# Kernel optimization log

Hardware: AMD Instinct MI355X
Metric: run time of the kernel (lower is better)

Reference implementation:

```python
import jax, jax.numpy as jnp
import numpy as np

D_MODEL = 256
N_HEADS = 8
D_FFN = 1024
B, N = 4, 1024
HEAD_DIM = D_MODEL // N_HEADS
LN_EPS = 1e-5


def _ln(x, g, b):
    mu = jnp.mean(x, axis=-1, keepdims=True)
    var = jnp.var(x, axis=-1, keepdims=True)
    return (x - mu) * jax.lax.rsqrt(var + LN_EPS) * g + b


def setup_inputs() -> dict:
    key = jax.random.key(0)
    ks = jax.random.split(key, 16)
    s = 0.02
    return {
        "embed": jax.random.normal(ks[0], (B, N, D_MODEL), jnp.float32),
        "refer_bbox": jax.random.uniform(ks[1], (B, N, 4), jnp.float32),
        "dist": jax.random.uniform(ks[2], (B, N, N), jnp.float32),
        "query_pos": jax.random.normal(ks[3], (B, N, D_MODEL), jnp.float32),
        "in_proj_w": jax.random.normal(ks[4], (3 * D_MODEL, D_MODEL), jnp.float32) * s,
        "in_proj_b": jnp.zeros((3 * D_MODEL,), jnp.float32),
        "out_w": jax.random.normal(ks[5], (D_MODEL, D_MODEL), jnp.float32) * s,
        "out_b": jnp.zeros((D_MODEL,), jnp.float32),
        "tau_w": jax.random.normal(ks[6], (N_HEADS, D_MODEL), jnp.float32) * s,
        "tau_b": jax.random.uniform(ks[7], (N_HEADS,), jnp.float32, 0.0, 2.0),
        "w1": jax.random.normal(ks[8], (D_FFN, D_MODEL), jnp.float32) * s,
        "b1": jnp.zeros((D_FFN,), jnp.float32),
        "w2": jax.random.normal(ks[9], (D_MODEL, D_FFN), jnp.float32) * s,
        "b2": jnp.zeros((D_MODEL,), jnp.float32),
        "g1": jnp.ones((D_MODEL,), jnp.float32),
        "beta1": jnp.zeros((D_MODEL,), jnp.float32),
        "g2": jnp.ones((D_MODEL,), jnp.float32),
        "beta2": jnp.zeros((D_MODEL,), jnp.float32),
    }


def reference(embed, refer_bbox, dist, query_pos, in_proj_w, in_proj_b, out_w, out_b,
              tau_w, tau_b, w1, b1, w2, b2, g1, beta1, g2, beta2):
    # tau: (B, N, H) -> (B, H, N); additive bias mask[b,h,i,j] = dist[b,i,j] * tau[b,h,i]
    tau = (embed @ tau_w.T + tau_b).transpose(0, 2, 1)
    bias = dist[:, None, :, :] * tau[..., None]  # (B, H, N, N)

    qk = embed + query_pos  # q = k = embed + pos, v = embed
    wq, wk, wv = jnp.split(in_proj_w, 3, axis=0)
    bq, bk, bv = jnp.split(in_proj_b, 3, axis=0)
    q = (qk @ wq.T + bq).reshape(B, N, N_HEADS, HEAD_DIM)
    k = (qk @ wk.T + bk).reshape(B, N, N_HEADS, HEAD_DIM)
    v = (embed @ wv.T + bv).reshape(B, N, N_HEADS, HEAD_DIM)

    scores = jnp.einsum("bihd,bjhd->bhij", q, k) / np.sqrt(HEAD_DIM) + bias
    attn = jax.nn.softmax(scores, axis=-1)
    ctx = jnp.einsum("bhij,bjhd->bihd", attn, v).reshape(B, N, D_MODEL)
    tgt = ctx @ out_w.T + out_b

    x = _ln(embed + tgt, g1, beta1)
    ffn = jax.nn.relu(x @ w1.T + b1) @ w2.T + b2
    return _ln(x + ffn, g2, beta2)
```

## Files before the change

kernel.cpp:

```cpp
#include <hip/hip_runtime.h>
#include <math.h>

#define D_MODEL 256
#define N_HEADS 8
#define HEAD_DIM 32
#define D_FFN   1024
#define BB      4
#define NN      1024
#define M_TOT   (BB * NN)
#define LN_EPS  1e-5f

#define QSCALE_LOG2E 0.2550348612f
#define LOG2E        1.4426950408889634f

typedef float f32x4 __attribute__((ext_vector_type(4)));
typedef short bf16x8 __attribute__((ext_vector_type(8)));

__device__ __forceinline__ unsigned short f2bf(float f) {
    unsigned int u = __float_as_uint(f);
    unsigned int r = (u + 0x7fffu + ((u >> 16) & 1u)) >> 16;
    return (unsigned short)r;
}
__device__ __forceinline__ ushort4 pack4(float4 v) {
    ushort4 o; o.x = f2bf(v.x); o.y = f2bf(v.y); o.z = f2bf(v.z); o.w = f2bf(v.w);
    return o;
}
__device__ __forceinline__ float fast_exp2(float x) {
#if __has_builtin(__builtin_amdgcn_exp2f)
    return __builtin_amdgcn_exp2f(x);
#else
    return exp2f(x);
#endif
}
__device__ __forceinline__ float bf2f(unsigned short s) {
    return __uint_as_float(((unsigned int)s) << 16);
}

__global__ __launch_bounds__(256)
void prep_all_kernel(const float4* __restrict__ e, const float4* __restrict__ qp,
                     ushort4* __restrict__ ebf, ushort4* __restrict__ qkbf,
                     const float4* __restrict__ inw, const float4* __restrict__ outw,
                     const float4* __restrict__ w1, const float4* __restrict__ w2,
                     const float4* __restrict__ tauw,
                     ushort4* __restrict__ o_inw, ushort4* __restrict__ o_outw,
                     ushort4* __restrict__ o_w1, ushort4* __restrict__ o_w2,
                     ushort4* __restrict__ o_taupad) {
    if (blockIdx.x < 1024) {
        int i = blockIdx.x * 256 + threadIdx.x;
        float4 ev = e[i], pv = qp[i];
        ebf[i] = pack4(ev);
        float4 s = make_float4(ev.x + pv.x, ev.y + pv.y, ev.z + pv.z, ev.w + pv.w);
        qkbf[i] = pack4(s);
    } else {
        int i = (blockIdx.x - 1024) * 256 + threadIdx.x;
        if (i < 49152)       o_inw[i] = pack4(inw[i]);
        else if (i < 65536)  o_outw[i - 49152] = pack4(outw[i - 49152]);
        else if (i < 131072) o_w1[i - 65536] = pack4(w1[i - 65536]);
        else if (i < 196608) o_w2[i - 131072] = pack4(w2[i - 131072]);
        else if (i < 200704) {
            int q = i - 196608;
            if (q < 512) o_taupad[q] = pack4(tauw[q]);
            else { ushort4 z = {0, 0, 0, 0}; o_taupad[q] = z; }
        }
    }
}

__global__ __launch_bounds__(256)
void qkv_mfma_kernel(const unsigned short* __restrict__ qk_bf,
                     const unsigned short* __restrict__ emb_bf,
                     const unsigned short* __restrict__ inw_bf,
                     const unsigned short* __restrict__ taupad,
                     const float* __restrict__ in_proj_b, const float* __restrict__ tau_b,
                     unsigned short* __restrict__ qb, unsigned short* __restrict__ kb,
                     unsigned short* __restrict__ vbT, float* __restrict__ taub) {
    __shared__ unsigned short vt[64][72];
    const int w    = threadIdx.x >> 6;
    const int lane = threadIdx.x & 63;
    const int l16 = lane & 15, l4 = lane >> 4;
    const int n0 = blockIdx.x * 64;
    const int m0 = blockIdx.y * 64;
    const int wm = (w >> 1) * 32, wn = (w & 1) * 32;
    const bool isv = (blockIdx.x >= 8) && (blockIdx.x < 12);

    const unsigned short* A = (blockIdx.x < 8) ? qk_bf : emb_bf;
    const unsigned short* W0 = (n0 < 768) ? &inw_bf[(size_t)(n0 + wn + l16) * D_MODEL]
                                          : &taupad[(size_t)(wn + l16) * D_MODEL];
    const unsigned short* Ar0 = &A[(size_t)(m0 + wm + l16) * D_MODEL];

    f32x4 acc[2][2] = {};
    #pragma unroll
    for (int k0 = 0; k0 < D_MODEL; k0 += 32) {
        bf16x8 a0 = *(const bf16x8*)&Ar0[k0 + l4 * 8];
        bf16x8 a1 = *(const bf16x8*)&Ar0[16 * D_MODEL + k0 + l4 * 8];
        bf16x8 b0 = *(const bf16x8*)&W0[k0 + l4 * 8];
        bf16x8 b1 = *(const bf16x8*)&W0[16 * D_MODEL + k0 + l4 * 8];
        acc[0][0] = __builtin_amdgcn_mfma_f32_16x16x32_bf16(a0, b0, acc[0][0], 0, 0, 0);
        acc[0][1] = __builtin_amdgcn_mfma_f32_16x16x32_bf16(a0, b1, acc[0][1], 0, 0, 0);
        acc[1][0] = __builtin_amdgcn_mfma_f32_16x16x32_bf16(a1, b0, acc[1][0], 0, 0, 0);
        acc[1][1] = __builtin_amdgcn_mfma_f32_16x16x32_bf16(a1, b1, acc[1][1], 0, 0, 0);
    }

    if (isv) {
        #pragma unroll
        for (int i = 0; i < 2; i++)
            #pragma unroll
            for (int j = 0; j < 2; j++) {
                const int cl = wn + j * 16 + l16;
                const float bs = in_proj_b[n0 + cl];
                #pragma unroll
                for (int r = 0; r < 4; r++)
                    vt[cl][wm + i * 16 + l4 * 4 + r] = f2bf(acc[i][j][r] + bs);
            }
        __syncthreads();
        const int t = threadIdx.x;
        const int cl = t >> 2, q4 = t & 3;
        const int cc = n0 + cl - 512;
        const int h = cc >> 5, d = cc & 31;
        const int b = m0 >> 10;
        const int nrow0 = (m0 & 1023) + q4 * 16;
        unsigned short* dst = &vbT[((size_t)(b * N_HEADS + h) * HEAD_DIM + d) * NN + nrow0];
        *(uint4*)dst       = *(const uint4*)&vt[cl][q4 * 16];
        *(uint4*)(dst + 8) = *(const uint4*)&vt[cl][q4 * 16 + 8];
        return;
    }

    #pragma unroll
    for (int i = 0; i < 2; i++) {
        #pragma unroll
        for (int j = 0; j < 2; j++) {
            #pragma unroll
            for (int r = 0; r < 4; r++) {
                const int m = m0 + wm + i * 16 + l4 * 4 + r;
                const int b = m >> 10, nrow = m & 1023;
                const int c = n0 + wn + j * 16 + l16;
                float v = acc[i][j][r];
                if (c < 256) {
                    v = (v + in_proj_b[c]) * QSCALE_LOG2E;
                    int h = c >> 5, d = c & 31;
                    qb[((size_t)(b * N_HEADS + h) * NN + nrow) * HEAD_DIM + d] = f2bf(v);
                } else if (c < 512) {
                    v += in_proj_b[c];
                    int cc = c - 256; int h = cc >> 5, d = cc & 31;
                    kb[((size_t)(b * N_HEADS + h) * NN + nrow) * HEAD_DIM + d] = f2bf(v);
                } else if (c < 776) {
                    v = (v + tau_b[c - 768]) * LOG2E;
                    taub[(size_t)(b * N_HEADS + (c - 768)) * NN + nrow] = v;
                }
            }
        }
    }
}

__global__ __launch_bounds__(256)
void attn_mfma_kernel(const unsigned short* __restrict__ qb,
                      const unsigned short* __restrict__ kb,
                      const unsigned short* __restrict__ vbT,
                      const float* __restrict__ taub,
                      const float* __restrict__ dist,
                      unsigned short* __restrict__ Opart,
                      float* __restrict__ lpart) {
    __shared__ unsigned short Kf[4][4][512];
    __shared__ unsigned short Vf[4][2][2][512];
    __shared__ unsigned short Plds[4][16 * 72];
    const int w    = threadIdx.x >> 6;
    const int lane = threadIdx.x & 63;
    const int l16  = lane & 15;
    const int l4   = lane >> 4;
    const int bh = blockIdx.y;
    const int b = bh >> 3;
    const int z = blockIdx.z;
    const int i0 = blockIdx.x * 64 + w * 16;
    const int jbase = z * 256;

    {
        const int kt = w;
        const unsigned short* kb_z = &kb[((size_t)bh * NN + jbase + kt * 64) * HEAD_DIM];
        #pragma unroll
        for (int s = 0; s < 4; s++) {
            bf16x8 kv = *(const bf16x8*)&kb_z[(size_t)(l16 * 4 + s) * HEAD_DIM + l4 * 8];
            *(bf16x8*)&Kf[kt][s][lane * 8] = kv;
        }
        const unsigned short* vb_z = &vbT[(size_t)bh * HEAD_DIM * NN + jbase + kt * 64];
        #pragma unroll
        for (int c = 0; c < 2; c++)
            #pragma unroll
            for (int h2 = 0; h2 < 2; h2++) {
                bf16x8 vv = *(const bf16x8*)&vb_z[(size_t)(h2 * 16 + l16) * NN + c * 32 + l4 * 8];
                *(bf16x8*)&Vf[kt][c][h2][lane * 8] = vv;
            }
    }

    const f32x4 zero = {0.f, 0.f, 0.f, 0.f};
    bf16x8 qf = *(const bf16x8*)&qb[((size_t)bh * NN + i0 + l16) * HEAD_DIM + l4 * 8];
    float tau_r[4];
    const float* drow[4];
    #pragma unroll
    for (int r = 0; r < 4; r++) {
        tau_r[r] = taub[(size_t)bh * NN + i0 + l4 * 4 + r];
        drow[r] = &dist[((size_t)b * NN + i0 + l4 * 4 + r) * NN + jbase];
    }
    float l_acc[4] = {0.f, 0.f, 0.f, 0.f};
    f32x4 O0 = zero, O1 = zero;
    unsigned short* pw = &Plds[w][0];

    __syncthreads();

    for (int kt = 0; kt < 4; kt++) {
        const int j0 = kt * 64;
        f32x4 dd4[4];
        #pragma unroll
        for (int r = 0; r < 4; r++)
            dd4[r] = *(const f32x4*)&drow[r][j0 + l16 * 4];

        float parr[4][4];
        #pragma unroll
        for (int s = 0; s < 4; s++) {
            bf16x8 kfr = *(const bf16x8*)&Kf[kt][s][lane * 8];
            f32x4 S = __builtin_amdgcn_mfma_f32_16x16x32_bf16(qf, kfr, zero, 0, 0, 0);
            #pragma unroll
            for (int r = 0; r < 4; r++) {
                const float p = fast_exp2(S[r] + dd4[r][s] * tau_r[r]);
                parr[s][r] = p;
                l_acc[r] += p;
            }
        }

        #pragma unroll
        for (int r = 0; r < 4; r++) {
            ushort4 pk;
            pk.x = f2bf(parr[0][r]); pk.y = f2bf(parr[1][r]);
            pk.z = f2bf(parr[2][r]); pk.w = f2bf(parr[3][r]);
            *(ushort4*)&pw[(l4 * 4 + r) * 72 + l16 * 4] = pk;
        }
        asm volatile("s_waitcnt lgkmcnt(0)" ::: "memory");
        #pragma unroll
        for (int c = 0; c < 2; c++) {
            bf16x8 pf = *(const bf16x8*)&pw[l16 * 72 + c * 32 + l4 * 8];
            bf16x8 v0 = *(const bf16x8*)&Vf[kt][c][0][lane * 8];
            bf16x8 v1 = *(const bf16x8*)&Vf[kt][c][1][lane * 8];
            O0 = __builtin_amdgcn_mfma_f32_16x16x32_bf16(pf, v0, O0, 0, 0, 0);
            O1 = __builtin_amdgcn_mfma_f32_16x16x32_bf16(pf, v1, O1, 0, 0, 0);
        }
    }

    #pragma unroll
    for (int msk = 1; msk < 16; msk <<= 1)
        #pragma unroll
        for (int r = 0; r < 4; r++)
            l_acc[r] += __shfl_xor(l_acc[r], msk, 16);

    #pragma unroll
    for (int r = 0; r < 4; r++) {
        const int i = i0 + l4 * 4 + r;
        unsigned short* crow = &Opart[((size_t)(z * 32 + bh) * NN + i) * 32];
        crow[l16]      = f2bf(O0[r]);
        crow[16 + l16] = f2bf(O1[r]);
        if (l16 == 0)
            lpart[(size_t)(z * 32 + bh) * NN + i] = l_acc[r];
    }
}

__global__ __launch_bounds__(1024)
void post_kernel(const unsigned short* __restrict__ Opart, const float* __restrict__ lpart,
                 const unsigned short* __restrict__ outw,
                 const float* __restrict__ out_b, const float* __restrict__ embed,
                 const float* __restrict__ g1, const float* __restrict__ beta1,
                 const unsigned short* __restrict__ w1, const float* __restrict__ b1,
                 const unsigned short* __restrict__ w2, const float* __restrict__ b2,
                 const float* __restrict__ g2, const float* __restrict__ beta2,
                 float* __restrict__ out) {
    __shared__ float Lh[16][8];
    __shared__ unsigned short cs[16][264];
    __shared__ unsigned short xs[16][264];
    __shared__ unsigned short fs[16][1032];
    __shared__ float sums[16][4][4][2];

    const int tid = threadIdx.x;
    const int w = tid >> 6, lane = tid & 63;
    const int l16 = lane & 15, l4 = lane >> 4;
    const int m0 = blockIdx.x * 16;
    const int b = m0 >> 10;

    if (tid < 128) {
        const int row = tid >> 3, h = tid & 7;
        const int i = (m0 + row) & 1023;
        const int rowA = ((b * 8 + h) << 10) + i;
        float l = 0.f;
        #pragma unroll
        for (int z = 0; z < 4; z++) l += lpart[z * 32768 + rowA];
        Lh[row][h] = 1.0f / l;
    }
    __syncthreads();

    {
        const int row = tid >> 6;
        const int d0 = (tid & 63) * 4;
        const int h = d0 >> 5;
        const int dd = d0 & 31;
        const int i = (m0 + row) & 1023;
        const int rowA = ((b * 8 + h) << 10) + i;
        float s[4] = {};
        #pragma unroll
        for (int z = 0; z < 4; z++) {
            ushort4 u = *(const ushort4*)&Opart[((size_t)(z * 32768 + rowA)) * 32 + dd];
            s[0] += bf2f(u.x); s[1] += bf2f(u.y); s[2] += bf2f(u.z); s[3] += bf2f(u.w);
        }
        const float li = Lh[row][h];
        ushort4 o;
        o.x = f2bf(s[0] * li); o.y = f2bf(s[1] * li);
        o.z = f2bf(s[2] * li); o.w = f2bf(s[3] * li);
        *(ushort4*)&cs[row][d0] = o;
    }
    __syncthreads();

    const int cA = w * 16 + l16;
    f32x4 a0 = {}, a1 = {};
    {
        const unsigned short* wr = &outw[(size_t)cA * D_MODEL];
        #pragma unroll
        for (int kk = 0; kk < 4; kk++) {
            const int k0 = kk * 32, k1 = 128 + kk * 32;
            bf16x8 x0 = *(const bf16x8*)&cs[l16][k0 + l4 * 8];
            bf16x8 b0 = *(const bf16x8*)&wr[k0 + l4 * 8];
            bf16x8 x1 = *(const bf16x8*)&cs[l16][k1 + l4 * 8];
            bf16x8 b1v = *(const bf16x8*)&wr[k1 + l4 * 8];
            a0 = __builtin_amdgcn_mfma_f32_16x16x32_bf16(x0, b0, a0, 0, 0, 0);
            a1 = __builtin_amdgcn_mfma_f32_16x16x32_bf16(x1, b1v, a1, 0, 0, 0);
        }
    }
    bf16x8 wf[4];
    #pragma unroll
    for (int j = 0; j < 4; j++)
        wf[j] = *(const bf16x8*)&w1[(size_t)(w * 64 + j * 16 + l16) * D_MODEL + l4 * 8];

    float xv[4];
    {
        float s_r[4] = {0.f, 0.f, 0.f, 0.f}, q_r[4] = {0.f, 0.f, 0.f, 0.f};
        const float bs = out_b[cA];
        #pragma unroll
        for (int r = 0; r < 4; r++) {
            const int m = m0 + l4 * 4 + r;
            const float t = a0[r] + a1[r] + bs + embed[(size_t)m * D_MODEL + cA];
            xv[r] = t; s_r[r] += t; q_r[r] += t * t;
        }
        #pragma unroll
        for (int msk = 1; msk < 16; msk <<= 1)
            #pragma unroll
            for (int r = 0; r < 4; r++) {
                s_r[r] += __shfl_xor(s_r[r], msk, 16);
                q_r[r] += __shfl_xor(q_r[r], msk, 16);
            }
        if (l16 == 0)
            #pragma unroll
            for (int r = 0; r < 4; r++) {
                sums[w][l4][r][0] = s_r[r];
                sums[w][l4][r][1] = q_r[r];
            }
    }
    __syncthreads();
    #pragma unroll
    for (int r = 0; r < 4; r++) {
        float s = 0.f, q = 0.f;
        #pragma unroll
        for (int ww = 0; ww < 16; ww++) { s += sums[ww][l4][r][0]; q += sums[ww][l4][r][1]; }
        const float mu = s * (1.0f / D_MODEL);
        const float var = q * (1.0f / D_MODEL) - mu * mu;
        const float rstd = rsqrtf(var + LN_EPS);
        const float ov = (xv[r] - mu) * rstd * g1[cA] + beta1[cA];
        xv[r] = ov;
        xs[l4 * 4 + r][cA] = f2bf(ov);
    }
    __syncthreads();

    f32x4 accB[4] = {};
    {
        bf16x8 wfn[4];
        #pragma unroll
        for (int kk = 0; kk < 8; kk++) {
            const int k0 = kk * 32;
            if (kk < 7) {
                #pragma unroll
                for (int j = 0; j < 4; j++)
                    wfn[j] = *(const bf16x8*)&w1[(size_t)(w * 64 + j * 16 + l16) * D_MODEL + k0 + 32 + l4 * 8];
            }
            bf16x8 a = *(const bf16x8*)&xs[l16][k0 + l4 * 8];
            #pragma unroll
            for (int j = 0; j < 4; j++)
                accB[j] = __builtin_amdgcn_mfma_f32_16x16x32_bf16(a, wf[j], accB[j], 0, 0, 0);
            if (kk < 7) {
                #pragma unroll
                for (int j = 0; j < 4; j++) wf[j] = wfn[j];
            }
        }
    }
    const unsigned short* wr2 = &w2[(size_t)cA * D_FFN];
    bf16x8 wb0 = *(const bf16x8*)&wr2[l4 * 8];
    bf16x8 wb1 = *(const bf16x8*)&wr2[512 + l4 * 8];

    #pragma unroll
    for (int j = 0; j < 4; j++) {
        const int fc = w * 64 + j * 16 + l16;
        const float bs = b1[fc];
        #pragma unroll
        for (int r = 0; r < 4; r++)
            fs[l4 * 4 + r][fc] = f2bf(fmaxf(accB[j][r] + bs, 0.f));
    }
    __syncthreads();

    f32x4 c0 = {}, c1 = {};
    {
        #pragma unroll
        for (int kk = 0; kk < 16; kk++) {
            const int k0 = kk * 32, k1 = 512 + kk * 32;
            bf16x8 cur0 = wb0, cur1 = wb1;
            if (kk < 15) {
                wb0 = *(const bf16x8*)&wr2[k0 + 32 + l4 * 8];
                wb1 = *(const bf16x8*)&wr2[k1 + 32 + l4 * 8];
            }
            bf16x8 f0 = *(const bf16x8*)&fs[l16][k0 + l4 * 8];
            bf16x8 f1 = *(const bf16x8*)&fs[l16][k1 + l4 * 8];
            c0 = __builtin_amdgcn_mfma_f32_16x16x32_bf16(f0, cur0, c0, 0, 0, 0);
            c1 = __builtin_amdgcn_mfma_f32_16x16x32_bf16(f1, cur1, c1, 0, 0, 0);
        }
    }
    float v2[4];
    {
        float s_r[4] = {0.f, 0.f, 0.f, 0.f}, q_r[4] = {0.f, 0.f, 0.f, 0.f};
        const float bs = b2[cA];
        #pragma unroll
        for (int r = 0; r < 4; r++) {
            const float t = c0[r] + c1[r] + bs + xv[r];
            v2[r] = t; s_r[r] += t; q_r[r] += t * t;
        }
        #pragma unroll
        for (int msk = 1; msk < 16; msk <<= 1)
            #pragma unroll
            for (int r = 0; r < 4; r++) {
                s_r[r] += __shfl_xor(s_r[r], msk, 16);
                q_r[r] += __shfl_xor(q_r[r], msk, 16);
            }
        if (l16 == 0)
            #pragma unroll
            for (int r = 0; r < 4; r++) {
                sums[w][l4][r][0] = s_r[r];
                sums[w][l4][r][1] = q_r[r];
            }
    }
    __syncthreads();
    #pragma unroll
    for (int r = 0; r < 4; r++) {
        float s = 0.f, q = 0.f;
        #pragma unroll
        for (int ww = 0; ww < 16; ww++) { s += sums[ww][l4][r][0]; q += sums[ww][l4][r][1]; }
        const float mu = s * (1.0f / D_MODEL);
        const float var = q * (1.0f / D_MODEL) - mu * mu;
        const float rstd = rsqrtf(var + LN_EPS);
        const int m = m0 + l4 * 4 + r;
        out[(size_t)m * D_MODEL + cA] = (v2[r] - mu) * rstd * g2[cA] + beta2[cA];
    }
}

extern "C" void kernel_launch(void* const* d_in, const int* in_sizes, int n_in,
                              void* d_out, int out_size, void* d_ws, size_t ws_size,
                              hipStream_t stream) {
    const float* embed     = (const float*)d_in[0];
    const float* dist      = (const float*)d_in[2];
    const float* query_pos = (const float*)d_in[3];
    const float* in_proj_w = (const float*)d_in[4];
    const float* in_proj_b = (const float*)d_in[5];
    const float* out_w     = (const float*)d_in[6];
    const float* out_b     = (const float*)d_in[7];
    const float* tau_w     = (const float*)d_in[8];
    const float* tau_b     = (const float*)d_in[9];
    const float* w1        = (const float*)d_in[10];
    const float* b1        = (const float*)d_in[11];
    const float* w2        = (const float*)d_in[12];
    const float* b2        = (const float*)d_in[13];
    const float* g1        = (const float*)d_in[14];
    const float* beta1     = (const float*)d_in[15];
    const float* g2        = (const float*)d_in[16];
    const float* beta2     = (const float*)d_in[17];
    float* out = (float*)d_out;

    char* ws = (char*)d_ws;
    const size_t MB = 1024 * 1024;
    const size_t KB = 1024;
    unsigned short* emb_bf  = (unsigned short*)(ws);
    unsigned short* qk_bf   = (unsigned short*)(ws + 2 * MB);
    unsigned short* qb      = (unsigned short*)(ws + 4 * MB);
    unsigned short* kb      = (unsigned short*)(ws + 6 * MB);
    unsigned short* vbT     = (unsigned short*)(ws + 8 * MB);
    float*          taub    = (float*)(ws + 10 * MB);
    unsigned short* inw_bf  = (unsigned short*)(ws + 11 * MB);
    unsigned short* outw_bf = (unsigned short*)(ws + 11 * MB + 512 * KB);
    unsigned short* w1_bf   = (unsigned short*)(ws + 12 * MB);
    unsigned short* w2_bf   = (unsigned short*)(ws + 12 * MB + 512 * KB);
    unsigned short* taupad  = (unsigned short*)(ws + 13 * MB);
    unsigned short* Opart   = (unsigned short*)(ws + 14 * MB);
    float*          lpart   = (float*)(ws + 22 * MB);

    prep_all_kernel<<<dim3(1808), dim3(256), 0, stream>>>(
        (const float4*)embed, (const float4*)query_pos,
        (ushort4*)emb_bf, (ushort4*)qk_bf,
        (const float4*)in_proj_w, (const float4*)out_w, (const float4*)w1,
        (const float4*)w2, (const float4*)tau_w,
        (ushort4*)inw_bf, (ushort4*)outw_bf, (ushort4*)w1_bf, (ushort4*)w2_bf,
        (ushort4*)taupad);

    qkv_mfma_kernel<<<dim3(13, M_TOT / 64), dim3(256), 0, stream>>>(
        qk_bf, emb_bf, inw_bf, taupad, in_proj_b, tau_b, qb, kb, vbT, taub);

    attn_mfma_kernel<<<dim3(NN / 64, BB * N_HEADS, 4), dim3(256), 0, stream>>>(
        qb, kb, vbT, taub, dist, Opart, lpart);

    post_kernel<<<dim3(M_TOT / 16), dim3(1024), 0, stream>>>(
        Opart, lpart, outw_bf, out_b, embed, g1, beta1,
        w1_bf, b1, w2_bf, b2, g2, beta2, out);
}
```

Before: 181.9 us.

## Convert dist to bf16 in prep and process two query tiles per attention wave

Adds a pass in the prep kernel that converts the full dist matrix (B·N·N floats) to bf16. The attention kernel then reads half as many bytes of dist for each of the 8 heads that reuse it. Each attention block now covers 128 query rows (two 16-row tiles per wave), so the K/V tiles loaded into LDS are reused twice and the grid is half as large. The cost is an extra full read of the fp32 dist and a bf16 write, a loss of precision in the distance bias, and more registers per thread.

```diff
diff --git a/kernel.cpp b/kernel.cpp
--- a/kernel.cpp
+++ b/kernel.cpp
@@ -44,14 +44,15 @@
                      const float4* __restrict__ tauw,
                      ushort4* __restrict__ o_inw, ushort4* __restrict__ o_outw,
                      ushort4* __restrict__ o_w1, ushort4* __restrict__ o_w2,
-                     ushort4* __restrict__ o_taupad) {
+                     ushort4* __restrict__ o_taupad,
+                     const float4* __restrict__ dist, ushort4* __restrict__ o_dist) {
     if (blockIdx.x < 1024) {
         int i = blockIdx.x * 256 + threadIdx.x;
         float4 ev = e[i], pv = qp[i];
         ebf[i] = pack4(ev);
         float4 s = make_float4(ev.x + pv.x, ev.y + pv.y, ev.z + pv.z, ev.w + pv.w);
         qkbf[i] = pack4(s);
-    } else {
+    } else if (blockIdx.x < 1808) {
         int i = (blockIdx.x - 1024) * 256 + threadIdx.x;
         if (i < 49152)       o_inw[i] = pack4(inw[i]);
         else if (i < 65536)  o_outw[i - 49152] = pack4(outw[i - 49152]);
@@ -62,6 +63,9 @@
             if (q < 512) o_taupad[q] = pack4(tauw[q]);
             else { ushort4 z = {0, 0, 0, 0}; o_taupad[q] = z; }
         }
+    } else {
+        int i = (blockIdx.x - 1808) * 256 + threadIdx.x;
+        o_dist[i] = pack4(dist[i]);
     }
 }
 
@@ -156,7 +160,7 @@
                       const unsigned short* __restrict__ kb,
                       const unsigned short* __restrict__ vbT,
                       const float* __restrict__ taub,
-                      const float* __restrict__ dist,
+                      const unsigned short* __restrict__ dist_bf,
                       unsigned short* __restrict__ Opart,
                       float* __restrict__ lpart) {
     __shared__ unsigned short Kf[4][4][512];
@@ -169,7 +173,6 @@
     const int bh = blockIdx.y;
     const int b = bh >> 3;
     const int z = blockIdx.z;
-    const int i0 = blockIdx.x * 64 + w * 16;
     const int jbase = z * 256;
 
     {
@@ -191,73 +194,91 @@
     }
 
     const f32x4 zero = {0.f, 0.f, 0.f, 0.f};
-    bf16x8 qf = *(const bf16x8*)&qb[((size_t)bh * NN + i0 + l16) * HEAD_DIM + l4 * 8];
-    float tau_r[4];
-    const float* drow[4];
-    #pragma unroll
-    for (int r = 0; r < 4; r++) {
-        tau_r[r] = taub[(size_t)bh * NN + i0 + l4 * 4 + r];
-        drow[r] = &dist[((size_t)b * NN + i0 + l4 * 4 + r) * NN + jbase];
-    }
-    float l_acc[4] = {0.f, 0.f, 0.f, 0.f};
-    f32x4 O0 = zero, O1 = zero;
+    int i0[2];
+    i0[0] = blockIdx.x * 128 + w * 16;
+    i0[1] = i0[0] + 64;
+
+    bf16x8 qf[2];
+    float tau_r[2][4];
+    const unsigned short* drow[2][4];
+    #pragma unroll
+    for (int t = 0; t < 2; t++) {
+        qf[t] = *(const bf16x8*)&qb[((size_t)bh * NN + i0[t] + l16) * HEAD_DIM + l4 * 8];
+        #pragma unroll
+        for (int r = 0; r < 4; r++) {
+            tau_r[t][r] = taub[(size_t)bh * NN + i0[t] + l4 * 4 + r];
+            drow[t][r] = &dist_bf[((size_t)b * NN + i0[t] + l4 * 4 + r) * NN + jbase];
+        }
+    }
+    float l_acc[2][4] = {};
+    f32x4 O0[2] = {zero, zero}, O1[2] = {zero, zero};
     unsigned short* pw = &Plds[w][0];
 
     __syncthreads();
 
     for (int kt = 0; kt < 4; kt++) {
         const int j0 = kt * 64;
-        f32x4 dd4[4];
-        #pragma unroll
-        for (int r = 0; r < 4; r++)
-            dd4[r] = *(const f32x4*)&drow[r][j0 + l16 * 4];
-
-        float parr[4][4];
-        #pragma unroll
-        for (int s = 0; s < 4; s++) {
-            bf16x8 kfr = *(const bf16x8*)&Kf[kt][s][lane * 8];
-            f32x4 S = __builtin_amdgcn_mfma_f32_16x16x32_bf16(qf, kfr, zero, 0, 0, 0);
-            #pragma unroll
-            for (int r = 0; r < 4; r++) {
-                const float p = fast_exp2(S[r] + dd4[r][s] * tau_r[r]);
-                parr[s][r] = p;
-                l_acc[r] += p;
-            }
-        }
-
+        #pragma unroll
+        for (int t = 0; t < 2; t++) {
+            float dd[4][4];
+            #pragma unroll
+            for (int r = 0; r < 4; r++) {
+                ushort4 du = *(const ushort4*)&drow[t][r][j0 + l16 * 4];
+                dd[r][0] = bf2f(du.x); dd[r][1] = bf2f(du.y);
+                dd[r][2] = bf2f(du.z); dd[r][3] = bf2f(du.w);
+            }
+
+            float parr[4][4];
+            #pragma unroll
+            for (int s = 0; s < 4; s++) {
+                bf16x8 kfr = *(const bf16x8*)&Kf[kt][s][lane * 8];
+                f32x4 S = __builtin_amdgcn_mfma_f32_16x16x32_bf16(qf[t], kfr, zero, 0, 0, 0);
+                #pragma unroll
+                for (int r = 0; r < 4; r++) {
+                    const float p = fast_exp2(S[r] + dd[r][s] * tau_r[t][r]);
+                    parr[s][r] = p;
+                    l_acc[t][r] += p;
+                }
+            }
+
+            #pragma unroll
+            for (int r = 0; r < 4; r++) {
+                ushort4 pk;
+                pk.x = f2bf(parr[0][r]); pk.y = f2bf(parr[1][r]);
+                pk.z = f2bf(parr[2][r]); pk.w = f2bf(parr[3][r]);
+                *(ushort4*)&pw[(l4 * 4 + r) * 72 + l16 * 4] = pk;
+            }
+            asm volatile("s_waitcnt lgkmcnt(0)" ::: "memory");
+            #pragma unroll
+            for (int c = 0; c < 2; c++) {
+                bf16x8 pf = *(const bf16x8*)&pw[l16 * 72 + c * 32 + l4 * 8];
+                bf16x8 v0 = *(const bf16x8*)&Vf[kt][c][0][lane * 8];
+                bf16x8 v1 = *(const bf16x8*)&Vf[kt][c][1][lane * 8];
+                O0[t] = __builtin_amdgcn_mfma_f32_16x16x32_bf16(pf, v0, O0[t], 0, 0, 0);
+                O1[t] = __builtin_amdgcn_mfma_f32_16x16x32_bf16(pf, v1, O1[t], 0, 0, 0);
+            }
+        }
+    }
+
+    #pragma unroll
+    for (int msk = 1; msk < 16; msk <<= 1)
+        #pragma unroll
+        for (int t = 0; t < 2; t++)
+            #pragma unroll
+            for (int r = 0; r < 4; r++)
+                l_acc[t][r] += __shfl_xor(l_acc[t][r], msk, 16);
+
+    #pragma unroll
+    for (int t = 0; t < 2; t++)
         #pragma unroll
         for (int r = 0; r < 4; r++) {
-            ushort4 pk;
-            pk.x = f2bf(parr[0][r]); pk.y = f2bf(parr[1][r]);
-            pk.z = f2bf(parr[2][r]); pk.w = f2bf(parr[3][r]);
-            *(ushort4*)&pw[(l4 * 4 + r) * 72 + l16 * 4] = pk;
-        }
-        asm volatile("s_waitcnt lgkmcnt(0)" ::: "memory");
-        #pragma unroll
-        for (int c = 0; c < 2; c++) {
-            bf16x8 pf = *(const bf16x8*)&pw[l16 * 72 + c * 32 + l4 * 8];
-            bf16x8 v0 = *(const bf16x8*)&Vf[kt][c][0][lane * 8];
-            bf16x8 v1 = *(const bf16x8*)&Vf[kt][c][1][lane * 8];
-            O0 = __builtin_amdgcn_mfma_f32_16x16x32_bf16(pf, v0, O0, 0, 0, 0);
-            O1 = __builtin_amdgcn_mfma_f32_16x16x32_bf16(pf, v1, O1, 0, 0, 0);
-        }
-    }
-
-    #pragma unroll
-    for (int msk = 1; msk < 16; msk <<= 1)
-        #pragma unroll
-        for (int r = 0; r < 4; r++)
-            l_acc[r] += __shfl_xor(l_acc[r], msk, 16);
-
-    #pragma unroll
-    for (int r = 0; r < 4; r++) {
-        const int i = i0 + l4 * 4 + r;
-        unsigned short* crow = &Opart[((size_t)(z * 32 + bh) * NN + i) * 32];
-        crow[l16]      = f2bf(O0[r]);
-        crow[16 + l16] = f2bf(O1[r]);
-        if (l16 == 0)
-            lpart[(size_t)(z * 32 + bh) * NN + i] = l_acc[r];
-    }
+            const int i = i0[t] + l4 * 4 + r;
+            unsigned short* crow = &Opart[((size_t)(z * 32 + bh) * NN + i) * 32];
+            crow[l16]      = f2bf(O0[t][r]);
+            crow[16 + l16] = f2bf(O1[t][r]);
+            if (l16 == 0)
+                lpart[(size_t)(z * 32 + bh) * NN + i] = l_acc[t][r];
+        }
 }
 
 __global__ __launch_bounds__(1024)
@@ -498,20 +519,21 @@
     unsigned short* taupad  = (unsigned short*)(ws + 13 * MB);
     unsigned short* Opart   = (unsigned short*)(ws + 14 * MB);
     float*          lpart   = (float*)(ws + 22 * MB);
-
-    prep_all_kernel<<<dim3(1808), dim3(256), 0, stream>>>(
+    unsigned short* dist_bf = (unsigned short*)(ws + 23 * MB);
+
+    prep_all_kernel<<<dim3(5904), dim3(256), 0, stream>>>(
         (const float4*)embed, (const float4*)query_pos,
         (ushort4*)emb_bf, (ushort4*)qk_bf,
         (const float4*)in_proj_w, (const float4*)out_w, (const float4*)w1,
         (const float4*)w2, (const float4*)tau_w,
         (ushort4*)inw_bf, (ushort4*)outw_bf, (ushort4*)w1_bf, (ushort4*)w2_bf,
-        (ushort4*)taupad);
+        (ushort4*)taupad, (const float4*)dist, (ushort4*)dist_bf);
 
     qkv_mfma_kernel<<<dim3(13, M_TOT / 64), dim3(256), 0, stream>>>(
         qk_bf, emb_bf, inw_bf, taupad, in_proj_b, tau_b, qb, kb, vbT, taub);
 
-    attn_mfma_kernel<<<dim3(NN / 64, BB * N_HEADS, 4), dim3(256), 0, stream>>>(
-        qb, kb, vbT, taub, dist, Opart, lpart);
+    attn_mfma_kernel<<<dim3(NN / 128, BB * N_HEADS, 4), dim3(256), 0, stream>>>(
+        qb, kb, vbT, taub, dist_bf, Opart, lpart);
 
     post_kernel<<<dim3(M_TOT / 16), dim3(1024), 0, stream>>>(
         Opart, lpart, outw_bf, out_b, embed, g1, beta1,
```

Result: no change. 184.5 us (+1.4%).
